# Optimization experiments

Hardware: AMD Instinct MI355X
Metric: run time of the kernel (lower is better)

Reference implementation:

```python
import jax, jax.numpy as jnp
import numpy as np

N_NODES = 16384
D_IN = 256
D_OUT = 256
AVG_DEG = 32


def setup_inputs() -> dict:
    key = jax.random.key(0)
    kx, ka, kw, kb = jax.random.split(key, 4)
    x = jax.random.normal(kx, (N_NODES, D_IN), dtype=jnp.float32)
    # Binary dense adjacency with average degree ~AVG_DEG (matches `adj[i] > 0` usage).
    adj = (jax.random.uniform(ka, (N_NODES, N_NODES)) < (AVG_DEG / N_NODES)).astype(jnp.float32)
    # nn.Linear(2*in_features, out_features): weight [out, 2*in], bias [out]
    W = jax.random.normal(kw, (D_OUT, 2 * D_IN), dtype=jnp.float32) * (1.0 / np.sqrt(2 * D_IN))
    b = jnp.zeros((D_OUT,), dtype=jnp.float32)
    return {"x": x, "adj": adj, "W": W, "b": b, "sample_size": 10}


def reference(x, adj, W, b, sample_size):
    # Vectorized equivalent of the per-node loop:
    # sample min(deg, sample_size) neighbors uniformly without replacement,
    # mean-aggregate, concat with self features, linear + relu.
    key = jax.random.key(42)
    noise = jax.random.uniform(key, adj.shape)            # [N, N]
    # Gumbel-top-k trick: top-k uniform scores over neighbors == uniform sample w/o replacement.
    scores = jnp.where(adj > 0, noise, -jnp.inf)
    top_scores, top_idx = jax.lax.top_k(scores, sample_size)  # [N, k]
    valid = jnp.isfinite(top_scores)                          # [N, k] false where deg < k
    feats = x[top_idx] * valid[..., None].astype(x.dtype)     # [N, k, d]
    cnt = valid.sum(axis=-1, keepdims=True).astype(x.dtype)   # [N, 1]
    agg = feats.sum(axis=1) / jnp.maximum(cnt, 1.0)           # mean; zeros if no neighbors
    h = jnp.concatenate([x, agg], axis=-1)                    # [N, 2d]
    return jax.nn.relu(h @ W.T + b)
```

## Files before the change

### kernel.cpp

```cpp
#include <hip/hip_runtime.h>
#include <hip/hip_bf16.h>
#include <stdint.h>

#define N_NODES 16384
#define D_IN    256
#define D_OUT   256
#define K_SAMP  10
#define HALF_FLAT (1u << 27)

#define JAX_PARTITIONABLE 1

__device__ __forceinline__ uint32_t rotl32(uint32_t x, int r) {
    return (x << r) | (x >> (32 - r));
}

__device__ __forceinline__ uint32_t jax_noise_bits(uint32_t r, uint32_t c) {
    const uint32_t i  = (r << 14) | c;
    const uint32_t k0 = 0u, k1 = 42u;
    const uint32_t k2 = 42u ^ 0x1BD11BDAu;
    uint32_t x0, x1;
#if JAX_PARTITIONABLE
    x0 = 0u;
    x1 = i;
#else
    const bool lo = (i < HALF_FLAT);
    x0 = lo ? i : (i - HALF_FLAT);
    x1 = lo ? (i + HALF_FLAT) : i;
#endif
    x0 += k0; x1 += k1;
#define TFR4(a,b,cc,d) \
    x0 += x1; x1 = rotl32(x1,a);  x1 ^= x0; \
    x0 += x1; x1 = rotl32(x1,b);  x1 ^= x0; \
    x0 += x1; x1 = rotl32(x1,cc); x1 ^= x0; \
    x0 += x1; x1 = rotl32(x1,d);  x1 ^= x0;
    TFR4(13,15,26,6);   x0 += k1; x1 += k2 + 1u;
    TFR4(17,29,16,24);  x0 += k2; x1 += k0 + 2u;
    TFR4(13,15,26,6);   x0 += k0; x1 += k1 + 3u;
    TFR4(17,29,16,24);  x0 += k1; x1 += k2 + 4u;
    TFR4(13,15,26,6);   x0 += k2; x1 += k0 + 5u;
#undef TFR4
#if JAX_PARTITIONABLE
    return x0 ^ x1;
#else
    return (i < HALF_FLAT) ? x0 : x1;
#endif
}

__device__ __forceinline__ unsigned short f2bfbits(float f) {
    __hip_bfloat16 h = __float2bfloat16(f);
    return *(unsigned short*)&h;
}

__global__ __launch_bounds__(256) void k_agg(
    const float* __restrict__ x, const float* __restrict__ adj,
    unsigned short* __restrict__ h)
{
    const int t    = threadIdx.x;
    const int lane = t & 63;
    const int w    = t >> 6;
    const int r    = blockIdx.x * 4 + w;

    __shared__ unsigned short candc[4][128];

    const float4* rowp = (const float4*)(adj + (size_t)r * N_NODES);
    int nc = 0;
    #pragma unroll 8
    for (int it = 0; it < 64; ++it) {
        float4 v = rowp[it * 64 + lane];
        int cb = (it * 64 + lane) * 4;
        float vv[4] = {v.x, v.y, v.z, v.w};
        #pragma unroll
        for (int j = 0; j < 4; ++j) {
            unsigned long long mask = __ballot(vv[j] != 0.0f);
            if (mask) {
                if (vv[j] != 0.0f) {
                    int below = __builtin_amdgcn_mbcnt_hi(
                        (uint32_t)(mask >> 32),
                        __builtin_amdgcn_mbcnt_lo((uint32_t)mask, 0));
                    int slot = nc + below;
                    if (slot < 128) candc[w][slot] = (unsigned short)(cb + j);
                }
                nc += __popcll(mask);
            }
        }
    }
    __syncthreads();
    if (nc > 128) nc = 128;

    unsigned long long k0 = 0ull, k1 = 0ull;
    if (lane < nc) {
        uint32_t c   = candc[w][lane];
        uint32_t u23 = jax_noise_bits((uint32_t)r, c) >> 9;
        k0 = ((((unsigned long long)u23) << 14) | (unsigned long long)(16383u - c)) + 1ull;
    }
    if (64 + lane < nc) {
        uint32_t c   = candc[w][64 + lane];
        uint32_t u23 = jax_noise_bits((uint32_t)r, c) >> 9;
        k1 = ((((unsigned long long)u23) << 14) | (unsigned long long)(16383u - c)) + 1ull;
    }

    const int m = nc < K_SAMP ? nc : K_SAMP;
    float4 acc = {0.f, 0.f, 0.f, 0.f};
    for (int s = 0; s < m; ++s) {
        unsigned long long my = k0 > k1 ? k0 : k1;
        #pragma unroll
        for (int o = 1; o < 64; o <<= 1) {
            unsigned long long other = __shfl_xor(my, o);
            if (other > my) my = other;
        }
        if (k0 == my) k0 = 0ull; else if (k1 == my) k1 = 0ull;
        const int col = 16383 - (int)((my - 1ull) & 0x3FFFull);
        float4 xv = *(const float4*)(x + (size_t)col * D_IN + lane * 4);
        acc.x += xv.x; acc.y += xv.y; acc.z += xv.z; acc.w += xv.w;
    }
    const float inv = (m > 0) ? 1.0f / (float)m : 0.0f;

    float4 sv = *(const float4*)(x + (size_t)r * D_IN + lane * 4);
    ushort4 us, ua;
    us.x = f2bfbits(sv.x);        us.y = f2bfbits(sv.y);
    us.z = f2bfbits(sv.z);        us.w = f2bfbits(sv.w);
    ua.x = f2bfbits(acc.x * inv); ua.y = f2bfbits(acc.y * inv);
    ua.z = f2bfbits(acc.z * inv); ua.w = f2bfbits(acc.w * inv);
    unsigned short* hr = h + (size_t)r * (2 * D_IN);
    *(ushort4*)(hr + lane * 4)         = us;
    *(ushort4*)(hr + D_IN + lane * 4)  = ua;
}

__global__ __launch_bounds__(256) void k_convw(const float* __restrict__ W,
                                               unsigned short* __restrict__ Wb)
{
    int i = (blockIdx.x * 256 + threadIdx.x) * 4;
    float4 v = *(const float4*)(W + i);
    ushort4 u;
    u.x = f2bfbits(v.x); u.y = f2bfbits(v.y); u.z = f2bfbits(v.z); u.w = f2bfbits(v.w);
    *(ushort4*)(Wb + i) = u;
}

typedef __attribute__((ext_vector_type(8))) short  bf16x8;
typedef __attribute__((ext_vector_type(4))) float  f32x4;
typedef __attribute__((ext_vector_type(4))) int    i32x4;

#define BM 128
#define BN 64
#define BK 64

__global__ __launch_bounds__(256) void k_gemm(
    const unsigned short* __restrict__ h, const unsigned short* __restrict__ Wb,
    const float* __restrict__ bias, float* __restrict__ out)
{
    __shared__ short As[BM * BK];
    __shared__ short Bs[BN * BK];

    const int t    = threadIdx.x;
    const int lane = t & 63;
    const int wv   = t >> 6;
    const int wr   = wv >> 1;
    const int wc   = wv & 1;
    const int m0   = blockIdx.x * BM;
    const int n0   = blockIdx.y * BN;
    const int lr   = lane & 15;
    const int lk   = lane >> 4;

    f32x4 acc[4][2] = {};

    const short* hA = (const short*)h;
    const short* wB = (const short*)Wb;

    for (int k0 = 0; k0 < 2 * D_IN; k0 += BK) {
        #pragma unroll
        for (int i = 0; i < 4; ++i) {
            int q = t + i * 256;
            int row = q >> 3, c16 = q & 7;
            i32x4 v = *(const i32x4*)(hA + (size_t)(m0 + row) * 512 + k0 + c16 * 8);
            int ba = (row * 128 + c16 * 16) ^ ((row & 7) << 4);
            *(i32x4*)((char*)As + ba) = v;
        }
        #pragma unroll
        for (int i = 0; i < 2; ++i) {
            int q = t + i * 256;
            int row = q >> 3, c16 = q & 7;
            i32x4 v = *(const i32x4*)(wB + (size_t)(n0 + row) * 512 + k0 + c16 * 8);
            int ba = (row * 128 + c16 * 16) ^ ((row & 7) << 4);
            *(i32x4*)((char*)Bs + ba) = v;
        }
        __syncthreads();

        #pragma unroll
        for (int kk = 0; kk < BK; kk += 32) {
            bf16x8 af[4], bfr[2];
            #pragma unroll
            for (int mi = 0; mi < 4; ++mi) {
                int row = wr * 64 + mi * 16 + lr;
                int ba = (row * 128 + (kk + lk * 8) * 2) ^ ((row & 7) << 4);
                af[mi] = *(const bf16x8*)((const char*)As + ba);
            }
            #pragma unroll
            for (int ni = 0; ni < 2; ++ni) {
                int row = wc * 32 + ni * 16 + lr;
                int ba = (row * 128 + (kk + lk * 8) * 2) ^ ((row & 7) << 4);
                bfr[ni] = *(const bf16x8*)((const char*)Bs + ba);
            }
            #pragma unroll
            for (int mi = 0; mi < 4; ++mi)
                #pragma unroll
                for (int ni = 0; ni < 2; ++ni)
                    acc[mi][ni] = __builtin_amdgcn_mfma_f32_16x16x32_bf16(
                        af[mi], bfr[ni], acc[mi][ni], 0, 0, 0);
        }
        __syncthreads();
    }

    #pragma unroll
    for (int mi = 0; mi < 4; ++mi) {
        #pragma unroll
        for (int ni = 0; ni < 2; ++ni) {
            int col = n0 + wc * 32 + ni * 16 + lr;
            float bv = bias[col];
            #pragma unroll
            for (int j = 0; j < 4; ++j) {
                int rowg = m0 + wr * 64 + mi * 16 + lk * 4 + j;
                float v = acc[mi][ni][j] + bv;
                out[(size_t)rowg * D_OUT + col] = v > 0.0f ? v : 0.0f;
            }
        }
    }
}

extern "C" void kernel_launch(void* const* d_in, const int* in_sizes, int n_in,
                              void* d_out, int out_size, void* d_ws, size_t ws_size,
                              hipStream_t stream) {
    (void)in_sizes; (void)n_in; (void)out_size; (void)ws_size;
    const float* x   = (const float*)d_in[0];
    const float* adj = (const float*)d_in[1];
    const float* W   = (const float*)d_in[2];
    const float* b   = (const float*)d_in[3];

    unsigned short* hbuf = (unsigned short*)d_ws;
    unsigned short* Wb   = (unsigned short*)((char*)d_ws + (size_t)N_NODES * 512 * 2);
    float* out = (float*)d_out;

    hipLaunchKernelGGL(k_convw, dim3((D_OUT * 2 * D_IN) / 1024), dim3(256), 0, stream, W, Wb);
    hipLaunchKernelGGL(k_agg,   dim3(N_NODES / 4), dim3(256), 0, stream, x, adj, hbuf);
    hipLaunchKernelGGL(k_gemm,  dim3(N_NODES / BM, D_OUT / BN), dim3(256), 0, stream,
                       hbuf, Wb, b, out);
}
```

Measured before the change: 241.8 us.

## Double-buffer GEMM LDS tiles, halve BM, and use nontemporal adj loads

The GEMM now uses 64x64 tiles with double-buffered LDS, prefetching the next K slice into registers while MFMAs run on the current buffer. This hides global load latency and doubles the number of blocks. The aggregation kernel reads the adjacency row with nontemporal loads so the streamed 1 GB matrix does not pollute the cache. The trade-off is more LDS per block and less reuse per tile, though the agg kernel dominates total time.

```diff
diff --git a/kernel.cpp b/kernel.cpp
--- a/kernel.cpp
+++ b/kernel.cpp
@@ -9,6 +9,10 @@
 #define HALF_FLAT (1u << 27)
 
 #define JAX_PARTITIONABLE 1
+
+typedef __attribute__((ext_vector_type(4))) float  f32x4;
+typedef __attribute__((ext_vector_type(8))) short  bf16x8;
+typedef __attribute__((ext_vector_type(4))) int    i32x4;
 
 __device__ __forceinline__ uint32_t rotl32(uint32_t x, int r) {
     return (x << r) | (x >> (32 - r));
@@ -62,18 +66,17 @@
 
     __shared__ unsigned short candc[4][128];
 
-    const float4* rowp = (const float4*)(adj + (size_t)r * N_NODES);
+    const f32x4* rowp = (const f32x4*)(adj + (size_t)r * N_NODES);
     int nc = 0;
     #pragma unroll 8
     for (int it = 0; it < 64; ++it) {
-        float4 v = rowp[it * 64 + lane];
+        f32x4 v = __builtin_nontemporal_load(rowp + it * 64 + lane);
         int cb = (it * 64 + lane) * 4;
-        float vv[4] = {v.x, v.y, v.z, v.w};
         #pragma unroll
         for (int j = 0; j < 4; ++j) {
-            unsigned long long mask = __ballot(vv[j] != 0.0f);
+            unsigned long long mask = __ballot(v[j] != 0.0f);
             if (mask) {
-                if (vv[j] != 0.0f) {
+                if (v[j] != 0.0f) {
                     int below = __builtin_amdgcn_mbcnt_hi(
                         (uint32_t)(mask >> 32),
                         __builtin_amdgcn_mbcnt_lo((uint32_t)mask, 0));
@@ -100,7 +103,7 @@
     }
 
     const int m = nc < K_SAMP ? nc : K_SAMP;
-    float4 acc = {0.f, 0.f, 0.f, 0.f};
+    f32x4 acc = {0.f, 0.f, 0.f, 0.f};
     for (int s = 0; s < m; ++s) {
         unsigned long long my = k0 > k1 ? k0 : k1;
         #pragma unroll
@@ -110,17 +113,17 @@
         }
         if (k0 == my) k0 = 0ull; else if (k1 == my) k1 = 0ull;
         const int col = 16383 - (int)((my - 1ull) & 0x3FFFull);
-        float4 xv = *(const float4*)(x + (size_t)col * D_IN + lane * 4);
-        acc.x += xv.x; acc.y += xv.y; acc.z += xv.z; acc.w += xv.w;
+        f32x4 xv = *(const f32x4*)(x + (size_t)col * D_IN + lane * 4);
+        acc += xv;
     }
     const float inv = (m > 0) ? 1.0f / (float)m : 0.0f;
 
-    float4 sv = *(const float4*)(x + (size_t)r * D_IN + lane * 4);
+    f32x4 sv = *(const f32x4*)(x + (size_t)r * D_IN + lane * 4);
     ushort4 us, ua;
-    us.x = f2bfbits(sv.x);        us.y = f2bfbits(sv.y);
-    us.z = f2bfbits(sv.z);        us.w = f2bfbits(sv.w);
-    ua.x = f2bfbits(acc.x * inv); ua.y = f2bfbits(acc.y * inv);
-    ua.z = f2bfbits(acc.z * inv); ua.w = f2bfbits(acc.w * inv);
+    us.x = f2bfbits(sv[0]);        us.y = f2bfbits(sv[1]);
+    us.z = f2bfbits(sv[2]);        us.w = f2bfbits(sv[3]);
+    ua.x = f2bfbits(acc[0] * inv); ua.y = f2bfbits(acc[1] * inv);
+    ua.z = f2bfbits(acc[2] * inv); ua.w = f2bfbits(acc[3] * inv);
     unsigned short* hr = h + (size_t)r * (2 * D_IN);
     *(ushort4*)(hr + lane * 4)         = us;
     *(ushort4*)(hr + D_IN + lane * 4)  = ua;
@@ -136,11 +139,7 @@
     *(ushort4*)(Wb + i) = u;
 }
 
-typedef __attribute__((ext_vector_type(8))) short  bf16x8;
-typedef __attribute__((ext_vector_type(4))) float  f32x4;
-typedef __attribute__((ext_vector_type(4))) int    i32x4;
-
-#define BM 128
+#define BM 64
 #define BN 64
 #define BK 64
 
@@ -148,8 +147,8 @@
     const unsigned short* __restrict__ h, const unsigned short* __restrict__ Wb,
     const float* __restrict__ bias, float* __restrict__ out)
 {
-    __shared__ short As[BM * BK];
-    __shared__ short Bs[BN * BK];
+    __shared__ short As[2][BM * BK];
+    __shared__ short Bs[2][BN * BK];
 
     const int t    = threadIdx.x;
     const int lane = t & 63;
@@ -161,64 +160,82 @@
     const int lr   = lane & 15;
     const int lk   = lane >> 4;
 
-    f32x4 acc[4][2] = {};
+    f32x4 acc[2][2] = {};
 
     const short* hA = (const short*)h;
     const short* wB = (const short*)Wb;
 
-    for (int k0 = 0; k0 < 2 * D_IN; k0 += BK) {
-        #pragma unroll
-        for (int i = 0; i < 4; ++i) {
-            int q = t + i * 256;
-            int row = q >> 3, c16 = q & 7;
-            i32x4 v = *(const i32x4*)(hA + (size_t)(m0 + row) * 512 + k0 + c16 * 8);
-            int ba = (row * 128 + c16 * 16) ^ ((row & 7) << 4);
-            *(i32x4*)((char*)As + ba) = v;
-        }
-        #pragma unroll
-        for (int i = 0; i < 2; ++i) {
-            int q = t + i * 256;
-            int row = q >> 3, c16 = q & 7;
-            i32x4 v = *(const i32x4*)(wB + (size_t)(n0 + row) * 512 + k0 + c16 * 8);
-            int ba = (row * 128 + c16 * 16) ^ ((row & 7) << 4);
-            *(i32x4*)((char*)Bs + ba) = v;
-        }
-        __syncthreads();
+    const int q0  = t, q1 = t + 256;
+    const int r0  = q0 >> 3, c0 = q0 & 7;
+    const int r1  = q1 >> 3, c1 = q1 & 7;
+    const int ba0 = (r0 * 128 + c0 * 16) ^ ((r0 & 7) << 4);
+    const int ba1 = (r1 * 128 + c1 * 16) ^ ((r1 & 7) << 4);
+
+    {
+        i32x4 a0 = *(const i32x4*)(hA + (size_t)(m0 + r0) * 512 + c0 * 8);
+        i32x4 a1 = *(const i32x4*)(hA + (size_t)(m0 + r1) * 512 + c1 * 8);
+        i32x4 b0 = *(const i32x4*)(wB + (size_t)(n0 + r0) * 512 + c0 * 8);
+        i32x4 b1 = *(const i32x4*)(wB + (size_t)(n0 + r1) * 512 + c1 * 8);
+        *(i32x4*)((char*)&As[0][0] + ba0) = a0;
+        *(i32x4*)((char*)&As[0][0] + ba1) = a1;
+        *(i32x4*)((char*)&Bs[0][0] + ba0) = b0;
+        *(i32x4*)((char*)&Bs[0][0] + ba1) = b1;
+    }
+    __syncthreads();
+
+    for (int tt = 0; tt < 8; ++tt) {
+        const int cur = tt & 1;
+        i32x4 a0, a1, b0, b1;
+        if (tt < 7) {
+            const int k0n = (tt + 1) * BK;
+            a0 = *(const i32x4*)(hA + (size_t)(m0 + r0) * 512 + k0n + c0 * 8);
+            a1 = *(const i32x4*)(hA + (size_t)(m0 + r1) * 512 + k0n + c1 * 8);
+            b0 = *(const i32x4*)(wB + (size_t)(n0 + r0) * 512 + k0n + c0 * 8);
+            b1 = *(const i32x4*)(wB + (size_t)(n0 + r1) * 512 + k0n + c1 * 8);
+        }
 
         #pragma unroll
         for (int kk = 0; kk < BK; kk += 32) {
-            bf16x8 af[4], bfr[2];
-            #pragma unroll
-            for (int mi = 0; mi < 4; ++mi) {
-                int row = wr * 64 + mi * 16 + lr;
+            bf16x8 af[2], bf[2];
+            #pragma unroll
+            for (int mi = 0; mi < 2; ++mi) {
+                int row = wr * 32 + mi * 16 + lr;
                 int ba = (row * 128 + (kk + lk * 8) * 2) ^ ((row & 7) << 4);
-                af[mi] = *(const bf16x8*)((const char*)As + ba);
+                af[mi] = *(const bf16x8*)((const char*)&As[cur][0] + ba);
             }
             #pragma unroll
             for (int ni = 0; ni < 2; ++ni) {
                 int row = wc * 32 + ni * 16 + lr;
                 int ba = (row * 128 + (kk + lk * 8) * 2) ^ ((row & 7) << 4);
-                bfr[ni] = *(const bf16x8*)((const char*)Bs + ba);
-            }
-            #pragma unroll
-            for (int mi = 0; mi < 4; ++mi)
+                bf[ni] = *(const bf16x8*)((const char*)&Bs[cur][0] + ba);
+            }
+            #pragma unroll
+            for (int mi = 0; mi < 2; ++mi)
                 #pragma unroll
                 for (int ni = 0; ni < 2; ++ni)
                     acc[mi][ni] = __builtin_amdgcn_mfma_f32_16x16x32_bf16(
-                        af[mi], bfr[ni], acc[mi][ni], 0, 0, 0);
+                        af[mi], bf[ni], acc[mi][ni], 0, 0, 0);
+        }
+
+        if (tt < 7) {
+            const int nxt = cur ^ 1;
+            *(i32x4*)((char*)&As[nxt][0] + ba0) = a0;
+            *(i32x4*)((char*)&As[nxt][0] + ba1) = a1;
+            *(i32x4*)((char*)&Bs[nxt][0] + ba0) = b0;
+            *(i32x4*)((char*)&Bs[nxt][0] + ba1) = b1;
         }
         __syncthreads();
     }
 
     #pragma unroll
-    for (int mi = 0; mi < 4; ++mi) {
+    for (int mi = 0; mi < 2; ++mi) {
         #pragma unroll
         for (int ni = 0; ni < 2; ++ni) {
             int col = n0 + wc * 32 + ni * 16 + lr;
             float bv = bias[col];
             #pragma unroll
             for (int j = 0; j < 4; ++j) {
-                int rowg = m0 + wr * 64 + mi * 16 + lk * 4 + j;
+                int rowg = m0 + wr * 32 + mi * 16 + lk * 4 + j;
                 float v = acc[mi][ni][j] + bv;
                 out[(size_t)rowg * D_OUT + col] = v > 0.0f ? v : 0.0f;
             }
```

New measurement: 220.0 us. -9.0%, faster.
